# Kernel optimization log

Measured on AMD Instinct MI355X. Metric: run time of the kernel, lower is better.

The kernel has to match this reference:

```python
import jax, jax.numpy as jnp
import numpy as np

N_NODES = 100000
N_EDGES = 1600000
NFEAT = 128
NHID = 64  # layer widths: NFEAT -> 2*NHID -> NHID


def setup_inputs() -> dict:
    key = jax.random.key(0)
    k_x, k_ei, k_ew, k_w1, k_b1, k_w2, k_b2 = jax.random.split(key, 7)
    x = jax.random.normal(k_x, (N_NODES, NFEAT), dtype=jnp.float32)
    edge_index = jax.random.randint(k_ei, (2, N_EDGES), 0, N_NODES, dtype=jnp.int64)
    edge_weight = jax.random.uniform(k_ew, (N_EDGES,), dtype=jnp.float32)
    h1 = 2 * NHID
    stdv1 = 1.0 / np.sqrt(h1)
    W1 = jax.random.uniform(k_w1, (NFEAT, h1), minval=-stdv1, maxval=stdv1, dtype=jnp.float32)
    b1 = jax.random.uniform(k_b1, (h1,), minval=-stdv1, maxval=stdv1, dtype=jnp.float32)
    stdv2 = 1.0 / np.sqrt(NHID)
    W2 = jax.random.uniform(k_w2, (h1, NHID), minval=-stdv2, maxval=stdv2, dtype=jnp.float32)
    b2 = jax.random.uniform(k_b2, (NHID,), minval=-stdv2, maxval=stdv2, dtype=jnp.float32)
    return {"x": x, "edge_index": edge_index, "edge_weight": edge_weight,
            "W1": W1, "b1": b1, "W2": W2, "b2": b2}


def reference(x, edge_index, edge_weight, W1, b1, W2, b2):
    # eval mode: dropout is identity; use_ln/layer_norm_first are False (defaults)
    src = edge_index[0]
    dst = edge_index[1]
    n = x.shape[0]

    def gcn_layer(h, W, b):
        support = h @ W                       # [N, F_out] dense transform
        msg = edge_weight[:, None] * support[src]  # [E, F_out] gather + scale
        agg = jax.ops.segment_sum(msg, dst, num_segments=n)  # scatter-add spmm
        return jax.nn.relu(agg + b)

    h = gcn_layer(x, W1, b1)   # NFEAT -> 2*NHID
    h = gcn_layer(h, W2, b2)   # 2*NHID -> NHID
    return h
```

## Files before the change

kernel.cpp:

```cpp
#include <hip/hip_runtime.h>


typedef __attribute__((ext_vector_type(8))) short bf16x8;
typedef __attribute__((ext_vector_type(4))) float f32x4;

#define CAPB 12288
#define PADCAP 4096

__device__ __forceinline__ ushort f2bf(float f) {
    uint u = __float_as_uint(f);
    u += 0x7fff + ((u >> 16) & 1);
    return (ushort)(u >> 16);
}
__device__ __forceinline__ float bf_lo(uint bits) { return __uint_as_float(bits << 16); }
__device__ __forceinline__ float bf_hi(uint bits) { return __uint_as_float(bits & 0xffff0000u); }

__global__ __launch_bounds__(256) void wconv_kernel(const float* __restrict__ W1,
                                                    ushort* __restrict__ Wt1,
                                                    const float* __restrict__ W2,
                                                    ushort* __restrict__ Wt2,
                                                    int* __restrict__ ccur) {
    if (blockIdx.x == 0) ccur[threadIdx.x] = 0;
    int i = blockIdx.x * 256 + threadIdx.x;
    if (i < 128 * 128) {
        int k = i >> 7, n = i & 127;
        Wt1[n * 128 + k] = f2bf(W1[i]);
    } else {
        int i2 = i - 128 * 128;
        if (i2 < 128 * 64) {
            int k = i2 >> 6, n = i2 & 63;
            Wt2[n * 128 + k] = f2bf(W2[i2]);
        }
    }
}

__device__ __forceinline__ void gemm1_body(const float* __restrict__ A,
                                           const ushort* __restrict__ Wt,
                                           ushort* __restrict__ C, int M,
                                           int rowblk, char* smem) {
    const int tid = threadIdx.x;
    const int m0 = rowblk * 128;

    #pragma unroll
    for (int it = 0; it < 8; ++it) {
        int c = tid + it * 256;
        int r = c >> 4;
        int k8 = (c & 15) << 3;
        int row = m0 + r;
        uint4 w4 = make_uint4(0u, 0u, 0u, 0u);
        if (row < M) {
            float4 v0 = *(const float4*)(A + (size_t)row * 128 + k8);
            float4 v1 = *(const float4*)(A + (size_t)row * 128 + k8 + 4);
            w4.x = (uint)f2bf(v0.x) | ((uint)f2bf(v0.y) << 16);
            w4.y = (uint)f2bf(v0.z) | ((uint)f2bf(v0.w) << 16);
            w4.z = (uint)f2bf(v1.x) | ((uint)f2bf(v1.y) << 16);
            w4.w = (uint)f2bf(v1.z) | ((uint)f2bf(v1.w) << 16);
        }
        int byte = (r * 256 + k8 * 2) ^ ((r & 7) << 4);
        *(uint4*)(smem + byte) = w4;
    }
    __syncthreads();

    const int wid = tid >> 6, lane = tid & 63;
    const int wy = wid >> 1;
    const int wx = wid & 1;
    const int rb = wy * 64;
    const int cb = wx * 64;
    const int ln = lane & 15;
    const int kg = lane >> 4;

    f32x4 acc[4][4];
    #pragma unroll
    for (int i = 0; i < 4; ++i)
        #pragma unroll
        for (int j = 0; j < 4; ++j) acc[i][j] = (f32x4){0.f, 0.f, 0.f, 0.f};

    #pragma unroll
    for (int s = 0; s < 4; ++s) {
        bf16x8 b[4];
        #pragma unroll
        for (int j = 0; j < 4; ++j)
            b[j] = *(const bf16x8*)(Wt + (size_t)(cb + j * 16 + ln) * 128 + s * 32 + kg * 8);
        bf16x8 a[4];
        #pragma unroll
        for (int i = 0; i < 4; ++i) {
            int r = rb + i * 16 + ln;
            int byte = (r * 256 + s * 64 + kg * 16) ^ ((r & 7) << 4);
            a[i] = *(const bf16x8*)(smem + byte);
        }
        #pragma unroll
        for (int i = 0; i < 4; ++i)
            #pragma unroll
            for (int j = 0; j < 4; ++j)
                acc[i][j] = __builtin_amdgcn_mfma_f32_16x16x32_bf16(a[i], b[j], acc[i][j], 0, 0, 0);
    }

    #pragma unroll
    for (int i = 0; i < 4; ++i)
        #pragma unroll
        for (int q = 0; q < 4; ++q) {
            int row = m0 + rb + i * 16 + kg * 4 + q;
            if (row < M) {
                #pragma unroll
                for (int j = 0; j < 4; ++j)
                    C[(size_t)row * 128 + cb + j * 16 + ln] = f2bf(acc[i][j][q]);
            }
        }
}

__device__ __forceinline__ void binA_body(const int* __restrict__ src,
                                          const int* __restrict__ dst,
                                          const float* __restrict__ ew,
                                          int* __restrict__ ccur,
                                          uint2* __restrict__ ebuf, int E,
                                          char* smem) {
    uint2* stage = (uint2*)smem;
    int* lh   = (int*)(smem + 32768);
    int* loff = (int*)(smem + 33792);
    int* gpos = (int*)(smem + 34816);
    unsigned char* sbuck = (unsigned char*)(smem + 35840);
    const int tid = threadIdx.x;
    const int base = blockIdx.x * 4096;
    const int nn = min(4096, E - base);

    lh[tid] = 0;
    __syncthreads();

    uint pk[16], wb[16];
    short bk[16], rk[16];
    #pragma unroll
    for (int i = 0; i < 16; ++i) {
        int li = tid + i * 256;
        bk[i] = -1;
        if (li < nn) {
            int e = base + li;
            int d = dst[e];
            int b = d >> 9;
            pk[i] = (uint)src[e] | ((uint)(d & 511) << 17);
            wb[i] = __float_as_uint(ew[e]);
            bk[i] = (short)b;
            rk[i] = (short)atomicAdd(&lh[b], 1);
        }
    }
    __syncthreads();

    int v = lh[tid];
    loff[tid] = v;
    __syncthreads();
    #pragma unroll
    for (int off = 1; off < 256; off <<= 1) {
        int t = (tid >= off) ? loff[tid - off] : 0;
        __syncthreads();
        loff[tid] += t;
        __syncthreads();
    }
    int excl = loff[tid] - v;
    __syncthreads();
    loff[tid] = excl;
    gpos[tid] = (v > 0) ? atomicAdd(&ccur[tid], v) : 0;
    __syncthreads();

    #pragma unroll
    for (int i = 0; i < 16; ++i)
        if (bk[i] >= 0) {
            int s = loff[bk[i]] + rk[i];
            stage[s] = make_uint2(pk[i], wb[i]);
            sbuck[s] = (unsigned char)bk[i];
        }
    __syncthreads();

    for (int s = tid; s < nn; s += 256) {
        uint2 e2 = stage[s];
        int b = sbuck[s];
        ebuf[(size_t)b * CAPB + gpos[b] + (s - loff[b])] = e2;
    }
}

__global__ __launch_bounds__(256) void fused_kernel(int csrB,
        const int* __restrict__ src, const int* __restrict__ dst,
        const float* __restrict__ ew, int* __restrict__ ccur,
        uint2* __restrict__ ebuf, int E,
        const float* __restrict__ x, const ushort* __restrict__ Wt1,
        ushort* __restrict__ S, int M) {
    __shared__ alignas(16) char smem[40960];
    if ((int)blockIdx.x < csrB)
        binA_body(src, dst, ew, ccur, ebuf, E, smem);
    else
        gemm1_body(x, Wt1, S, M, (int)blockIdx.x - csrB, smem);
}

__global__ __launch_bounds__(256) void gemm_mfma64(const ushort* __restrict__ Av,
                                                   const ushort* __restrict__ Wt,
                                                   ushort* __restrict__ C, int M) {
    __shared__ ushort As[128 * 128];
    const int tid = threadIdx.x;
    const int m0 = blockIdx.x * 128;

    #pragma unroll
    for (int it = 0; it < 8; ++it) {
        int c = tid + it * 256;
        int r = c >> 4;
        int k8 = (c & 15) << 3;
        int row = m0 + r;
        uint4 w4 = make_uint4(0u, 0u, 0u, 0u);
        if (row < M)
            w4 = *(const uint4*)(Av + (size_t)row * 128 + k8);
        int byte = (r * 256 + k8 * 2) ^ ((r & 7) << 4);
        *(uint4*)((char*)As + byte) = w4;
    }
    __syncthreads();

    const int wid = tid >> 6, lane = tid & 63;
    const int rb = wid * 32;
    const int ln = lane & 15;
    const int kg = lane >> 4;

    f32x4 acc[2][4];
    #pragma unroll
    for (int i = 0; i < 2; ++i)
        #pragma unroll
        for (int j = 0; j < 4; ++j) acc[i][j] = (f32x4){0.f, 0.f, 0.f, 0.f};

    #pragma unroll
    for (int s = 0; s < 4; ++s) {
        bf16x8 b[4];
        #pragma unroll
        for (int j = 0; j < 4; ++j)
            b[j] = *(const bf16x8*)(Wt + (size_t)(j * 16 + ln) * 128 + s * 32 + kg * 8);
        bf16x8 a[2];
        #pragma unroll
        for (int i = 0; i < 2; ++i) {
            int r = rb + i * 16 + ln;
            int byte = (r * 256 + s * 64 + kg * 16) ^ ((r & 7) << 4);
            a[i] = *(const bf16x8*)((const char*)As + byte);
        }
        #pragma unroll
        for (int i = 0; i < 2; ++i)
            #pragma unroll
            for (int j = 0; j < 4; ++j)
                acc[i][j] = __builtin_amdgcn_mfma_f32_16x16x32_bf16(a[i], b[j], acc[i][j], 0, 0, 0);
    }

    #pragma unroll
    for (int i = 0; i < 2; ++i)
        #pragma unroll
        for (int q = 0; q < 4; ++q) {
            int row = m0 + rb + i * 16 + kg * 4 + q;
            if (row < M) {
                #pragma unroll
                for (int j = 0; j < 4; ++j)
                    C[(size_t)row * 64 + j * 16 + ln] = f2bf(acc[i][j][q]);
            }
        }
}

__global__ __launch_bounds__(512) void binB_kernel(const uint2* __restrict__ ebuf,
                                                   const int* __restrict__ ccur,
                                                   int* __restrict__ rstart,
                                                   int* __restrict__ pdeg,
                                                   int2* __restrict__ csr, int N) {
    __shared__ int fh[512];
    __shared__ int pp[512];
    __shared__ int cur[512];
    const int c = blockIdx.x;
    const int tid = threadIdx.x;
    const int n0 = c << 9;
    const int cbase = c * CAPB;
    const int cend = cbase + ccur[c];
    const int pbase = c * (CAPB + PADCAP);

    fh[tid] = 0;
    __syncthreads();
    for (int e = cbase + tid; e < cend; e += 512)
        atomicAdd(&fh[ebuf[e].x >> 17], 1);
    __syncthreads();

    int cnt = fh[tid];
    int p = (cnt + 7) & ~7;
    pp[tid] = p;
    __syncthreads();
    #pragma unroll
    for (int off = 1; off < 512; off <<= 1) {
        int t = (tid >= off) ? pp[tid - off] : 0;
        __syncthreads();
        pp[tid] += t;
        __syncthreads();
    }
    int r = pbase + pp[tid] - p;
    if (n0 + tid < N) {
        rstart[n0 + tid] = r;
        pdeg[n0 + tid] = p;
    }
    cur[tid] = r;
    __syncthreads();

    for (int e = cbase + tid; e < cend; e += 512) {
        uint2 u = ebuf[e];
        int fine = u.x >> 17;
        int pos = atomicAdd(&cur[fine], 1);
        csr[pos] = make_int2((int)(u.x & 0x1FFFF), (int)u.y);
    }
    __syncthreads();

    for (int k = cur[tid]; k < r + p; ++k)
        csr[k] = make_int2(0, 0);
}

template <int F, int NPW, bool OBF>
__global__ __launch_bounds__(256) void agg_kernel(const ushort* __restrict__ sup,
                                                  const int* __restrict__ rstart,
                                                  const int* __restrict__ pdeg,
                                                  const int2* __restrict__ csr,
                                                  const float* __restrict__ bias,
                                                  void* __restrict__ outp, int N) {
    constexpr int LPN = 64 / NPW;
    constexpr int LPR = F / 8;
    static_assert(LPN / LPR == 2, "two slot-groups per node");
    const int lane = threadIdx.x & 63;
    const int wbase = ((blockIdx.x * 256 + threadIdx.x) >> 6) * NPW;
    if (wbase >= N) return;
    const int sub = lane / LPN;
    const int grp = (lane % LPN) / LPR;
    const int cl  = lane % LPR;
    const int node = wbase + sub;
    const bool nvalid = node < N;
    const int nidx = nvalid ? node : 0;
    const int rs = rstart[nidx];
    const int pd = nvalid ? pdeg[nidx] : 0;

    int pmax = pd;
    #pragma unroll
    for (int off = LPN; off < 64; off <<= 1)
        pmax = max(pmax, __shfl_xor(pmax, off));
    pmax = __builtin_amdgcn_readfirstlane(pmax);

    const ushort* rp = sup + cl * 8;
    float acc[8] = {0.f, 0.f, 0.f, 0.f, 0.f, 0.f, 0.f, 0.f};

    for (int j = 0; j < pmax; j += 16) {
        int2 m[8];
        #pragma unroll
        for (int t = 0; t < 8; ++t) {
            int slot = j + t * 2 + grp;
            bool ok = slot < pd;
            m[t] = csr[rs + (ok ? slot : 0)];
            if (!ok) m[t].y = 0;
        }
        uint4 v[8];
        #pragma unroll
        for (int t = 0; t < 8; ++t)
            v[t] = *(const uint4*)(rp + (size_t)m[t].x * F);
        #pragma unroll
        for (int t = 0; t < 8; ++t) {
            float w = __int_as_float(m[t].y);
            uint4 q = v[t];
            acc[0] = fmaf(bf_lo(q.x), w, acc[0]); acc[1] = fmaf(bf_hi(q.x), w, acc[1]);
            acc[2] = fmaf(bf_lo(q.y), w, acc[2]); acc[3] = fmaf(bf_hi(q.y), w, acc[3]);
            acc[4] = fmaf(bf_lo(q.z), w, acc[4]); acc[5] = fmaf(bf_hi(q.z), w, acc[5]);
            acc[6] = fmaf(bf_lo(q.w), w, acc[6]); acc[7] = fmaf(bf_hi(q.w), w, acc[7]);
        }
    }

    #pragma unroll
    for (int i = 0; i < 8; ++i) acc[i] += __shfl_xor(acc[i], LPR);

    if (grp == 0 && nvalid) {
        float4 b0 = ((const float4*)bias)[cl * 2 + 0];
        float4 b1 = ((const float4*)bias)[cl * 2 + 1];
        acc[0] = fmaxf(acc[0] + b0.x, 0.f); acc[1] = fmaxf(acc[1] + b0.y, 0.f);
        acc[2] = fmaxf(acc[2] + b0.z, 0.f); acc[3] = fmaxf(acc[3] + b0.w, 0.f);
        acc[4] = fmaxf(acc[4] + b1.x, 0.f); acc[5] = fmaxf(acc[5] + b1.y, 0.f);
        acc[6] = fmaxf(acc[6] + b1.z, 0.f); acc[7] = fmaxf(acc[7] + b1.w, 0.f);
        if (OBF) {
            uint4 o;
            o.x = (uint)f2bf(acc[0]) | ((uint)f2bf(acc[1]) << 16);
            o.y = (uint)f2bf(acc[2]) | ((uint)f2bf(acc[3]) << 16);
            o.z = (uint)f2bf(acc[4]) | ((uint)f2bf(acc[5]) << 16);
            o.w = (uint)f2bf(acc[6]) | ((uint)f2bf(acc[7]) << 16);
            ((uint4*)outp)[(size_t)node * LPR + cl] = o;
        } else {
            ((float4*)outp)[(size_t)node * LPR * 2 + cl * 2 + 0] =
                make_float4(acc[0], acc[1], acc[2], acc[3]);
            ((float4*)outp)[(size_t)node * LPR * 2 + cl * 2 + 1] =
                make_float4(acc[4], acc[5], acc[6], acc[7]);
        }
    }
}

extern "C" void kernel_launch(void* const* d_in, const int* in_sizes, int n_in,
                              void* d_out, int out_size, void* d_ws, size_t ws_size,
                              hipStream_t stream) {
    const float* x  = (const float*)d_in[0];
    const int*   ei = (const int*)d_in[1];
    const float* ew = (const float*)d_in[2];
    const float* W1 = (const float*)d_in[3];
    const float* b1 = (const float*)d_in[4];
    const float* W2 = (const float*)d_in[5];
    const float* b2 = (const float*)d_in[6];
    float* out = (float*)d_out;

    const int N = in_sizes[0] / 128;
    const int E = in_sizes[2];
    const int* src = ei;
    const int* dst = ei + E;
    const int NCB = (N + 511) / 512;
    const int GB = (N + 127) / 128;
    const int NBA = (E + 4095) / 4096;

    char* ws = (char*)d_ws;
    size_t o = 0;
    ushort* S      = (ushort*)(ws + o); o += (size_t)N * 128 * sizeof(ushort);
    ushort* H1b    = (ushort*)(ws + o); o += (size_t)N * 128 * sizeof(ushort);
    uint2*  ebuf   = (uint2*) (ws + o); o += (size_t)NCB * CAPB * sizeof(uint2);
    int2*   csr    = (int2*)  (ws + o); o += (size_t)NCB * (CAPB + PADCAP) * sizeof(int2);
    int*    rstart = (int*)   (ws + o); o += (size_t)N * sizeof(int);
    int*    pdeg   = (int*)   (ws + o); o += (size_t)N * sizeof(int);
    int*    ccur   = (int*)   (ws + o); o += 256 * sizeof(int);
    ushort* Wt1    = (ushort*)(ws + o); o += 128 * 128 * sizeof(ushort);
    ushort* Wt2    = (ushort*)(ws + o); o += 128 * 64 * sizeof(ushort);

    wconv_kernel<<<96, 256, 0, stream>>>(W1, Wt1, W2, Wt2, ccur);

    fused_kernel<<<NBA + GB, 256, 0, stream>>>(NBA, src, dst, ew, ccur,
                                               ebuf, E, x, Wt1, S, N);
    binB_kernel<<<NCB, 512, 0, stream>>>(ebuf, ccur, rstart, pdeg, csr, N);

    agg_kernel<128, 2, true><<<(N + 7) / 8, 256, 0, stream>>>(S, rstart, pdeg, csr, b1, H1b, N);

    gemm_mfma64<<<GB, 256, 0, stream>>>(H1b, Wt2, S, N);
    agg_kernel<64, 4, false><<<(N + 15) / 16, 256, 0, stream>>>(S, rstart, pdeg, csr, b2, out, N);
}
```

Measured before the change: 162.7 us.

## Overlap second GEMM on first-layer rows with remaining layer-1 aggregation

Splits the layer-1 aggregation into two parts. The first 60% of rows are aggregated first, then a fused launch runs the aggregation of the remaining rows alongside the layer-2 GEMM on the rows already finished. The GEMM on the remaining row tiles runs in a separate launch afterwards. The GEMM output goes to a separate buffer that reuses the edge bucket space, so it does not overwrite S while the tail aggregation still reads it. This aims to fill idle CUs and hide the GEMM behind the memory-bound aggregation, at the cost of one extra launch.

```diff
diff --git a/kernel.cpp b/kernel.cpp
--- a/kernel.cpp
+++ b/kernel.cpp
@@ -189,12 +189,12 @@
         gemm1_body(x, Wt1, S, M, (int)blockIdx.x - csrB, smem);
 }
 
-__global__ __launch_bounds__(256) void gemm_mfma64(const ushort* __restrict__ Av,
-                                                   const ushort* __restrict__ Wt,
-                                                   ushort* __restrict__ C, int M) {
-    __shared__ ushort As[128 * 128];
+__device__ __forceinline__ void gemm2_body(const ushort* __restrict__ Av,
+                                           const ushort* __restrict__ Wt,
+                                           ushort* __restrict__ C, int M,
+                                           int rowblk, char* smem) {
     const int tid = threadIdx.x;
-    const int m0 = blockIdx.x * 128;
+    const int m0 = rowblk * 128;
 
     #pragma unroll
     for (int it = 0; it < 8; ++it) {
@@ -206,7 +206,7 @@
         if (row < M)
             w4 = *(const uint4*)(Av + (size_t)row * 128 + k8);
         int byte = (r * 256 + k8 * 2) ^ ((r & 7) << 4);
-        *(uint4*)((char*)As + byte) = w4;
+        *(uint4*)(smem + byte) = w4;
     }
     __syncthreads();
 
@@ -232,7 +232,7 @@
         for (int i = 0; i < 2; ++i) {
             int r = rb + i * 16 + ln;
             int byte = (r * 256 + s * 64 + kg * 16) ^ ((r & 7) << 4);
-            a[i] = *(const bf16x8*)((const char*)As + byte);
+            a[i] = *(const bf16x8*)(smem + byte);
         }
         #pragma unroll
         for (int i = 0; i < 2; ++i)
@@ -252,6 +252,14 @@
                     C[(size_t)row * 64 + j * 16 + ln] = f2bf(acc[i][j][q]);
             }
         }
+}
+
+__global__ __launch_bounds__(256) void gemm2_kernel(const ushort* __restrict__ Av,
+                                                    const ushort* __restrict__ Wt,
+                                                    ushort* __restrict__ C, int M,
+                                                    int gOff) {
+    __shared__ alignas(16) char smem[32768];
+    gemm2_body(Av, Wt, C, M, gOff + (int)blockIdx.x, smem);
 }
 
 __global__ __launch_bounds__(512) void binB_kernel(const uint2* __restrict__ ebuf,
@@ -307,24 +315,25 @@
 }
 
 template <int F, int NPW, bool OBF>
-__global__ __launch_bounds__(256) void agg_kernel(const ushort* __restrict__ sup,
-                                                  const int* __restrict__ rstart,
-                                                  const int* __restrict__ pdeg,
-                                                  const int2* __restrict__ csr,
-                                                  const float* __restrict__ bias,
-                                                  void* __restrict__ outp, int N) {
+__device__ __forceinline__ void agg_body(const ushort* __restrict__ sup,
+                                         const int* __restrict__ rstart,
+                                         const int* __restrict__ pdeg,
+                                         const int2* __restrict__ csr,
+                                         const float* __restrict__ bias,
+                                         void* __restrict__ outp,
+                                         int n0, int n1, int bid) {
     constexpr int LPN = 64 / NPW;
     constexpr int LPR = F / 8;
     static_assert(LPN / LPR == 2, "two slot-groups per node");
     const int lane = threadIdx.x & 63;
-    const int wbase = ((blockIdx.x * 256 + threadIdx.x) >> 6) * NPW;
-    if (wbase >= N) return;
+    const int wbase = n0 + ((bid * 256 + (int)threadIdx.x) >> 6) * NPW;
+    if (wbase >= n1) return;
     const int sub = lane / LPN;
     const int grp = (lane % LPN) / LPR;
     const int cl  = lane % LPR;
     const int node = wbase + sub;
-    const bool nvalid = node < N;
-    const int nidx = nvalid ? node : 0;
+    const bool nvalid = node < n1;
+    const int nidx = nvalid ? node : n0;
     const int rs = rstart[nidx];
     const int pd = nvalid ? pdeg[nidx] : 0;
 
@@ -387,6 +396,29 @@
     }
 }
 
+template <int F, int NPW, bool OBF>
+__global__ __launch_bounds__(256) void agg_kernel(const ushort* __restrict__ sup,
+                                                  const int* __restrict__ rstart,
+                                                  const int* __restrict__ pdeg,
+                                                  const int2* __restrict__ csr,
+                                                  const float* __restrict__ bias,
+                                                  void* __restrict__ outp,
+                                                  int n0, int n1) {
+    agg_body<F, NPW, OBF>(sup, rstart, pdeg, csr, bias, outp, n0, n1, (int)blockIdx.x);
+}
+
+__global__ __launch_bounds__(256) void fused_tail(int aggB, int NA, int N,
+        const ushort* __restrict__ S, const int* __restrict__ rstart,
+        const int* __restrict__ pdeg, const int2* __restrict__ csr,
+        const float* __restrict__ b1, ushort* __restrict__ H1b,
+        const ushort* __restrict__ Wt2, ushort* __restrict__ S2) {
+    __shared__ alignas(16) char smem[32768];
+    if ((int)blockIdx.x < aggB)
+        agg_body<128, 2, true>(S, rstart, pdeg, csr, b1, H1b, NA, N, (int)blockIdx.x);
+    else
+        gemm2_body(H1b, Wt2, S2, N, (int)blockIdx.x - aggB, smem);
+}
+
 extern "C" void kernel_launch(void* const* d_in, const int* in_sizes, int n_in,
                               void* d_out, int out_size, void* d_ws, size_t ws_size,
                               hipStream_t stream) {
@@ -418,6 +450,11 @@
     int*    ccur   = (int*)   (ws + o); o += 256 * sizeof(int);
     ushort* Wt1    = (ushort*)(ws + o); o += 128 * 128 * sizeof(ushort);
     ushort* Wt2    = (ushort*)(ws + o); o += 128 * 64 * sizeof(ushort);
+    ushort* S2     = (ushort*)ebuf;
+
+    const int NA = ((N * 3 / 5) / 128) * 128;
+    const int TA = NA / 128;
+    const int aggB = (N - NA + 7) / 8;
 
     wconv_kernel<<<96, 256, 0, stream>>>(W1, Wt1, W2, Wt2, ccur);
 
@@ -425,8 +462,12 @@
                                                ebuf, E, x, Wt1, S, N);
     binB_kernel<<<NCB, 512, 0, stream>>>(ebuf, ccur, rstart, pdeg, csr, N);
 
-    agg_kernel<128, 2, true><<<(N + 7) / 8, 256, 0, stream>>>(S, rstart, pdeg, csr, b1, H1b, N);
-
-    gemm_mfma64<<<GB, 256, 0, stream>>>(H1b, Wt2, S, N);
-    agg_kernel<64, 4, false><<<(N + 15) / 16, 256, 0, stream>>>(S, rstart, pdeg, csr, b2, out, N);
-}
+    agg_kernel<128, 2, true><<<NA / 8, 256, 0, stream>>>(S, rstart, pdeg, csr,
+                                                         b1, H1b, 0, NA);
+    fused_tail<<<aggB + TA, 256, 0, stream>>>(aggB, NA, N, S, rstart, pdeg, csr,
+                                              b1, H1b, Wt2, S2);
+    gemm2_kernel<<<GB - TA, 256, 0, stream>>>(H1b, Wt2, S2, N, TA);
+
+    agg_kernel<64, 4, false><<<(N + 15) / 16, 256, 0, stream>>>(S2, rstart, pdeg,
+                                                                csr, b2, out, 0, N);
+}
```

New measurement: 171.9 us. +5.7%, slower.
